# Kernel optimization log

Hardware: AMD Instinct MI355X
Metric: run time of the kernel (lower is better)

The kernel has to match this reference:

```python
import jax, jax.numpy as jnp
import numpy as np
from functools import partial

H = 128  # GRU hidden size
L = 16   # dim_latents


def _gru_dir(x_tbd, W_ih, W_hh, b_ih, b_hh):
    """Single-direction GRU over time-major input x_tbd [T,B,D] -> [T,B,H].
    Torch gate order: r, z, n."""
    T, B, _ = x_tbd.shape
    # Precompute input projections for all timesteps: [T,B,3H]
    xp = jnp.einsum('tbd,gd->tbg', x_tbd, W_ih) + b_ih
    h0 = jnp.zeros((B, H), dtype=x_tbd.dtype)

    def step(h, xp_t):
        gh = h @ W_hh.T + b_hh            # [B,3H]
        xr, xz, xn = jnp.split(xp_t, 3, axis=-1)
        hr, hz, hn = jnp.split(gh, 3, axis=-1)
        r = jax.nn.sigmoid(xr + hr)
        z = jax.nn.sigmoid(xz + hz)
        n = jnp.tanh(xn + r * hn)
        h_new = (1.0 - z) * n + z * h
        return h_new, h_new

    _, ys = jax.lax.scan(step, h0, xp)
    return ys  # [T,B,H]


def setup_inputs() -> dict:
    key = jax.random.key(0)
    ks = jax.random.split(key, 8)
    B, T, N = 256, 1000, 256
    s_ih = 1.0 / np.sqrt(N)
    s_hh = 1.0 / np.sqrt(H)
    s_fc = 1.0 / np.sqrt(2 * H + L)
    return {
        'y_aux': jax.random.normal(ks[0], (B, T, N), dtype=jnp.float32),
        'W_ih_fwd': jax.random.normal(ks[1], (3 * H, N), dtype=jnp.float32) * s_ih,
        'W_hh_fwd': jax.random.normal(ks[2], (3 * H, H), dtype=jnp.float32) * s_hh,
        'b_ih_fwd': jnp.zeros((3 * H,), dtype=jnp.float32),
        'b_hh_fwd': jnp.zeros((3 * H,), dtype=jnp.float32),
        'W_ih_bwd': jax.random.normal(ks[3], (3 * H, N), dtype=jnp.float32) * s_ih,
        'W_hh_bwd': jax.random.normal(ks[4], (3 * H, H), dtype=jnp.float32) * s_hh,
        'b_ih_bwd': jnp.zeros((3 * H,), dtype=jnp.float32),
        'b_hh_bwd': jnp.zeros((3 * H,), dtype=jnp.float32),
        'W_mu': jax.random.normal(ks[5], (L, 2 * H + L), dtype=jnp.float32) * s_fc,
        'b_mu': jnp.zeros((L,), dtype=jnp.float32),
        'W_lv': jax.random.normal(ks[6], (L, 2 * H + L), dtype=jnp.float32) * s_fc,
        'b_lv': jnp.zeros((L,), dtype=jnp.float32),
    }


def reference(y_aux, W_ih_fwd, W_hh_fwd, b_ih_fwd, b_hh_fwd,
              W_ih_bwd, W_hh_bwd, b_ih_bwd, b_hh_bwd,
              W_mu, b_mu, W_lv, b_lv):
    # [B,T,N] -> time-major [T,B,N]
    x = jnp.transpose(y_aux, (1, 0, 2))
    out_f = _gru_dir(x, W_ih_fwd, W_hh_fwd, b_ih_fwd, b_hh_fwd)
    out_b = _gru_dir(x[::-1], W_ih_bwd, W_hh_bwd, b_ih_bwd, b_hh_bwd)[::-1]
    rnn_output = jnp.concatenate([out_f, out_b], axis=-1)  # [T,B,2H]
    # hn[0]: bidirectional hidden states at t=0
    hn0 = rnn_output[0]                                    # [B,2H]
    B = hn0.shape[0]
    temp = jnp.concatenate([jnp.zeros((B, L), dtype=hn0.dtype), hn0], axis=1)
    mu_0 = temp @ W_mu.T + b_mu
    log_var_0 = temp @ W_lv.T + b_lv
    return (mu_0, log_var_0, rnn_output)
```

## Files before the change

kernel.cpp:

```cpp
#include <hip/hip_runtime.h>
#include <hip/hip_bf16.h>

typedef short bf16x8 __attribute__((ext_vector_type(8)));
typedef float f32x4  __attribute__((ext_vector_type(4)));

#define TSTEPS 1000
#define BATCH  256
#define NIN    256
#define HID    128
#define TC     50
#define LOG2E  1.44269504088896f

#define GIDX_N 8192
#define XP4_ELEMS (2ull*TSTEPS*GIDX_N)
#define XP2_OFF_BYTES (XP4_ELEMS*16ull)
#define XP_NEED (XP4_ELEMS*16ull + 2ull*TSTEPS*GIDX_N*8ull)

__device__ __forceinline__ ushort f2bf(float f){
  union { float f; unsigned u; } v; v.f = f;
  unsigned r = v.u + 0x7fffu + ((v.u >> 16) & 1u);
  return (ushort)(r >> 16);
}
__device__ __forceinline__ uint pk2(float lo, float hi){
  __hip_bfloat162 h = __float22bfloat162_rn(make_float2(lo, hi));
  union { __hip_bfloat162 h; uint u; } c; c.h = h; return c.u;
}
__device__ __forceinline__ float bflo(uint w){ union{uint u;float f;}c; c.u = w<<16; return c.f; }
__device__ __forceinline__ float bfhi(uint w){ union{uint u;float f;}c; c.u = w & 0xffff0000u; return c.f; }

__device__ __forceinline__ float sigmoid_fast(float x){
  return __builtin_amdgcn_rcpf(1.f + __expf(-x));
}
__device__ __forceinline__ float tanh_fast(float a){
  const float e = __expf(2.f*fabsf(a));
  const float t = fmaf(-2.f, __builtin_amdgcn_rcpf(e + 1.f), 1.f);
  return copysignf(t, a);
}
__device__ __forceinline__ bf16x8 ld_w8(const float* p){
  union { uint u[4]; bf16x8 v; } c;
  c.u[0]=pk2(p[0],p[1]); c.u[1]=pk2(p[2],p[3]);
  c.u[2]=pk2(p[4],p[5]); c.u[3]=pk2(p[6],p[7]);
  return c.v;
}
__device__ __forceinline__ bf16x8 ld_w8s(const float* p, float s){
  union { uint u[4]; bf16x8 v; } c;
  c.u[0]=pk2(p[0]*s,p[1]*s); c.u[1]=pk2(p[2]*s,p[3]*s);
  c.u[2]=pk2(p[4]*s,p[5]*s); c.u[3]=pk2(p[6]*s,p[7]*s);
  return c.v;
}

__global__ __launch_bounds__(512) void xp_gemm(
    const float* __restrict__ y_aux,
    const float* __restrict__ Wf, const float* __restrict__ bihf, const float* __restrict__ bhhf,
    const float* __restrict__ Wb, const float* __restrict__ bihb, const float* __restrict__ bhhb,
    uint4* __restrict__ xp4, uint2* __restrict__ xp2)
{
  const int nch = TSTEPS/TC;
  const int blk = blockIdx.x;
  const int dir = blk / (16*nch);
  const int rem = blk % (16*nch);
  const int btile = rem / nch;
  const int tch = rem % nch;
  const int b0 = btile*16;
  const int tid=threadIdx.x, wave=tid>>6, lane=tid&63, lrow=lane&15, lgrp=lane>>4;
  const float* Wih = dir? Wb : Wf;
  const float* bih = dir? bihb : bihf;
  const float* bhh = dir? bhhb : bhhf;

  __shared__ __align__(16) ushort xsh[2][16][264];

  bf16x8 wf[3][8];
  f32x4 cinit[3];
  #pragma unroll
  for (int t3=0;t3<3;++t3){
    const int g = t3*128 + wave*16 + lrow;
    #pragma unroll
    for (int kk=0;kk<8;++kk)
      wf[t3][kk] = ld_w8s(Wih + g*NIN + kk*32 + lgrp*8, LOG2E);
    const float bv = LOG2E * (bih[g] + (t3<2 ? bhh[g] : 0.f));
    cinit[t3][0]=bv; cinit[t3][1]=bv; cinit[t3][2]=bv; cinit[t3][3]=bv;
  }

  const int row = tid>>5, f8 = tid&31;
  const float* xsrc = y_aux + (size_t)(b0+row)*(TSTEPS*NIN) + (size_t)(tch*TC)*NIN + f8*8;
  {
    float4 a = *(const float4*)xsrc;
    float4 b = *(const float4*)(xsrc+4);
    union{uint u[4]; bf16x8 v;} c;
    c.u[0]=pk2(a.x,a.y); c.u[1]=pk2(a.z,a.w); c.u[2]=pk2(b.x,b.y); c.u[3]=pk2(b.z,b.w);
    *(bf16x8*)&xsh[0][row][f8*8] = c.v;
  }
  float4 Aa = *(const float4*)(xsrc + 1*NIN), Ab = *(const float4*)(xsrc + 1*NIN + 4);
  float4 Ba = *(const float4*)(xsrc + 2*NIN), Bb = *(const float4*)(xsrc + 2*NIN + 4);
  __syncthreads();

  size_t sidx = ((size_t)dir*TSTEPS + (size_t)(tch*TC))*GIDX_N
              + (size_t)((btile*8 + wave)*64 + lane);

  for (int k=0;k<TC;k+=2){
    {
      f32x4 a0=cinit[0], a1=cinit[1], a2=cinit[2];
      #pragma unroll
      for (int kk=0;kk<8;++kk){
        bf16x8 a = *(const bf16x8*)&xsh[0][lrow][kk*32 + lgrp*8];
        a0 = __builtin_amdgcn_mfma_f32_16x16x32_bf16(a, wf[0][kk], a0, 0,0,0);
        a1 = __builtin_amdgcn_mfma_f32_16x16x32_bf16(a, wf[1][kk], a1, 0,0,0);
        a2 = __builtin_amdgcn_mfma_f32_16x16x32_bf16(a, wf[2][kk], a2, 0,0,0);
      }
      uint4 o4; o4.x=pk2(a0[0],a0[1]); o4.y=pk2(a0[2],a0[3]);
                o4.z=pk2(a1[0],a1[1]); o4.w=pk2(a1[2],a1[3]);
      uint2 o2; o2.x=pk2(a2[0],a2[1]); o2.y=pk2(a2[2],a2[3]);
      xp4[sidx]=o4; xp2[sidx]=o2; sidx += GIDX_N;
      union{uint u[4]; bf16x8 v;} c;
      c.u[0]=pk2(Aa.x,Aa.y); c.u[1]=pk2(Aa.z,Aa.w); c.u[2]=pk2(Ab.x,Ab.y); c.u[3]=pk2(Ab.z,Ab.w);
      *(bf16x8*)&xsh[1][row][f8*8] = c.v;
      const int t3 = (k+3 <= TC-1) ? (k+3) : (TC-1);
      Aa = *(const float4*)(xsrc + (size_t)t3*NIN);
      Ab = *(const float4*)(xsrc + (size_t)t3*NIN + 4);
      asm volatile("s_waitcnt lgkmcnt(0)\n\ts_barrier" ::: "memory");
    }
    {
      f32x4 a0=cinit[0], a1=cinit[1], a2=cinit[2];
      #pragma unroll
      for (int kk=0;kk<8;++kk){
        bf16x8 a = *(const bf16x8*)&xsh[1][lrow][kk*32 + lgrp*8];
        a0 = __builtin_amdgcn_mfma_f32_16x16x32_bf16(a, wf[0][kk], a0, 0,0,0);
        a1 = __builtin_amdgcn_mfma_f32_16x16x32_bf16(a, wf[1][kk], a1, 0,0,0);
        a2 = __builtin_amdgcn_mfma_f32_16x16x32_bf16(a, wf[2][kk], a2, 0,0,0);
      }
      uint4 o4; o4.x=pk2(a0[0],a0[1]); o4.y=pk2(a0[2],a0[3]);
                o4.z=pk2(a1[0],a1[1]); o4.w=pk2(a1[2],a1[3]);
      uint2 o2; o2.x=pk2(a2[0],a2[1]); o2.y=pk2(a2[2],a2[3]);
      xp4[sidx]=o4; xp2[sidx]=o2; sidx += GIDX_N;
      union{uint u[4]; bf16x8 v;} c;
      c.u[0]=pk2(Ba.x,Ba.y); c.u[1]=pk2(Ba.z,Ba.w); c.u[2]=pk2(Bb.x,Bb.y); c.u[3]=pk2(Bb.z,Bb.w);
      *(bf16x8*)&xsh[0][row][f8*8] = c.v;
      const int t4 = (k+4 <= TC-1) ? (k+4) : (TC-1);
      Ba = *(const float4*)(xsrc + (size_t)t4*NIN);
      Bb = *(const float4*)(xsrc + (size_t)t4*NIN + 4);
      asm volatile("s_waitcnt lgkmcnt(0)\n\ts_barrier" ::: "memory");
    }
  }
}

__global__ __launch_bounds__(512) void gru_rec(
    const uint4* __restrict__ xp4, const uint2* __restrict__ xp2,
    const float* __restrict__ Whhf, const float* __restrict__ bhhf,
    const float* __restrict__ Whhb, const float* __restrict__ bhhb,
    float* __restrict__ out)
{
  const int blk=blockIdx.x, dir=blk>>4, btile=blk&15, b0=btile<<4;
  const int tid=threadIdx.x, wave=tid>>6, lane=tid&63, lrow=lane&15, lgrp=lane>>4;
  const float* Whh = dir? Whhb : Whhf;
  const float* bhh = dir? bhhb : bhhf;

  __shared__ __align__(16) ushort hbuf[2][16][136];

  bf16x8 whh[3][4];
  #pragma unroll
  for (int t3=0;t3<3;++t3){
    const int g = t3*128 + wave*16 + lrow;
    #pragma unroll
    for (int kk=0;kk<4;++kk)
      whh[t3][kk] = ld_w8s(Whh + g*HID + kk*32 + lgrp*8, LOG2E);
  }
  const int hcol = wave*16 + lrow;
  const float bh2s = LOG2E * bhh[256 + hcol];

  { ushort* hb=&hbuf[0][0][0]; for (int i=tid;i<16*136;i+=512) hb[i]=0; }

  const int tt0 = dir? (TSTEPS-1):0;
  const long long d4 = dir? -(long long)GIDX_N : (long long)GIDX_N;
  const size_t gbase = ((size_t)dir*TSTEPS + (size_t)tt0)*GIDX_N
                     + (size_t)((btile*8+wave)*64+lane);
  const uint4* q4p = xp4 + gbase;
  const uint2* q2p = xp2 + gbase;
  uint4 q40 = q4p[0], q41 = q4p[d4];
  uint2 q20 = q2p[0], q21 = q2p[d4];
  const uint4* f4 = q4p + 2*d4;
  const uint2* f2 = q2p + 2*d4;

  float* op = out + 8192 + (size_t)tt0*(BATCH*2*HID)
            + (size_t)(b0 + lgrp*4)*(2*HID) + dir*HID + hcol;
  const long long odel = dir? -(long long)(BATCH*2*HID) : (long long)(BATCH*2*HID);

  float hm[4]={0,0,0,0};
  __syncthreads();

  for (int s=0;s<TSTEPS;++s){
    const int cur=s&1, nxt=cur^1;
    uint4 q42 = *f4; f4 += d4;
    uint2 q22 = *f2; f2 += d4;

    f32x4 ar={0,0,0,0}, az={0,0,0,0}, an={0,0,0,0};
    #pragma unroll
    for (int kk=0;kk<4;++kk){
      bf16x8 a = *(const bf16x8*)&hbuf[cur][lrow][kk*32 + lgrp*8];
      ar = __builtin_amdgcn_mfma_f32_16x16x32_bf16(a, whh[0][kk], ar, 0,0,0);
      az = __builtin_amdgcn_mfma_f32_16x16x32_bf16(a, whh[1][kk], az, 0,0,0);
      an = __builtin_amdgcn_mfma_f32_16x16x32_bf16(a, whh[2][kk], an, 0,0,0);
    }

    float hv[4];
    {
      const float xr[4] = {bflo(q40.x),bfhi(q40.x),bflo(q40.y),bfhi(q40.y)};
      const float xz[4] = {bflo(q40.z),bfhi(q40.z),bflo(q40.w),bfhi(q40.w)};
      const float xn[4] = {bflo(q20.x),bfhi(q20.x),bflo(q20.y),bfhi(q20.y)};
      #pragma unroll
      for (int i=0;i<4;++i){
        const float r = __builtin_amdgcn_rcpf(1.f + __builtin_amdgcn_exp2f(-(ar[i]+xr[i])));
        const float z = __builtin_amdgcn_rcpf(1.f + __builtin_amdgcn_exp2f(-(az[i]+xz[i])));
        const float y  = fmaf(r, an[i]+bh2s, xn[i]);
        const float y2 = y + y;
        const float e  = __builtin_amdgcn_exp2f(fabsf(y2));
        const float t  = fmaf(-2.f, __builtin_amdgcn_rcpf(e+1.f), 1.f);
        const float n  = copysignf(t, y);
        hv[i] = fmaf(z, hm[i]-n, n);
        hm[i] = hv[i];
      }
    }
    const uint p01 = pk2(hv[0],hv[1]);
    const uint p23 = pk2(hv[2],hv[3]);
    hbuf[nxt][lgrp*4+0][hcol] = (ushort)p01;
    hbuf[nxt][lgrp*4+1][hcol] = (ushort)(p01>>16);
    hbuf[nxt][lgrp*4+2][hcol] = (ushort)p23;
    hbuf[nxt][lgrp*4+3][hcol] = (ushort)(p23>>16);
    op[0]   = hv[0];
    op[256] = hv[1];
    op[512] = hv[2];
    op[768] = hv[3];
    op += odel;
    q40=q41; q41=q42; q20=q21; q21=q22;
    asm volatile("s_waitcnt lgkmcnt(0)\n\ts_barrier" ::: "memory");
  }
}

__global__ __launch_bounds__(512) void gru_fused(
    const float* __restrict__ y_aux,
    const float* __restrict__ W_ih_f, const float* __restrict__ W_hh_f,
    const float* __restrict__ b_ih_f, const float* __restrict__ b_hh_f,
    const float* __restrict__ W_ih_b, const float* __restrict__ W_hh_b,
    const float* __restrict__ b_ih_b, const float* __restrict__ b_hh_b,
    float* __restrict__ out)
{
  const int blk  = blockIdx.x;
  const int dir  = blk >> 4;
  const int b0   = (blk & 15) << 4;
  const int tid  = threadIdx.x;
  const int wave = tid >> 6;
  const int lane = tid & 63;
  const int lrow = lane & 15;
  const int lgrp = lane >> 4;

  const float* Wih = dir ? W_ih_b : W_ih_f;
  const float* Whh = dir ? W_hh_b : W_hh_f;
  const float* bih = dir ? b_ih_b : b_ih_f;
  const float* bhh = dir ? b_hh_b : b_hh_f;

  __shared__ __align__(16) ushort hbuf[2][16][136];
  __shared__ __align__(16) ushort xbuf[2][16][264];

  bf16x8 wih_f[3][8];
  bf16x8 whh_f[3][4];
  #pragma unroll
  for (int t3 = 0; t3 < 3; ++t3){
    const int g = t3*128 + wave*16 + lrow;
    #pragma unroll
    for (int kk = 0; kk < 8; ++kk) wih_f[t3][kk] = ld_w8(Wih + g*NIN + kk*32 + lgrp*8);
    #pragma unroll
    for (int kk = 0; kk < 4; ++kk) whh_f[t3][kk] = ld_w8(Whh + g*HID + kk*32 + lgrp*8);
  }
  float bihv[3], bhhv[3];
  #pragma unroll
  for (int t3 = 0; t3 < 3; ++t3){
    const int g = t3*128 + wave*16 + lrow;
    bihv[t3] = bih[g];
    bhhv[t3] = bhh[g];
  }

  for (int i = tid; i < 2*16*136; i += 512) ((ushort*)hbuf)[i] = 0;
  {
    const int row = tid >> 5, f8 = tid & 31;
    const int t0  = dir ? (TSTEPS-1) : 0;
    const float* p = y_aux + (size_t)(b0+row)*(TSTEPS*NIN) + (size_t)t0*NIN + f8*8;
    union{uint u[4]; bf16x8 v;} c;
    float4 a = *(const float4*)p; float4 b = *(const float4*)(p+4);
    c.u[0]=pk2(a.x,a.y); c.u[1]=pk2(a.z,a.w); c.u[2]=pk2(b.x,b.y); c.u[3]=pk2(b.z,b.w);
    *(bf16x8*)&xbuf[0][row][f8*8] = c.v;
  }
  __syncthreads();

  float hm[4] = {0.f, 0.f, 0.f, 0.f};
  const int hcol = wave*16 + lrow;
  float* outr = out + 8192;

  for (int s = 0; s < TSTEPS; ++s){
    const int tt  = dir ? (TSTEPS-1-s) : s;
    const int cur = s & 1, nxt = cur ^ 1;
    const int tn   = dir ? (tt-1) : (tt+1);
    const int prow = tid >> 5, pf8 = tid & 31;
    const bool more = (s < TSTEPS-1);
    float4 pa, pb;
    if (more){
      const float* p = y_aux + (size_t)(b0+prow)*(TSTEPS*NIN) + (size_t)tn*NIN + pf8*8;
      pa = *(const float4*)p;
      pb = *(const float4*)(p+4);
    }

    f32x4 a_rh = {0,0,0,0}, a_zh = {0,0,0,0}, a_nh = {0,0,0,0};
    f32x4 a_rx = {0,0,0,0}, a_zx = {0,0,0,0}, a_nx = {0,0,0,0};
    #pragma unroll
    for (int kk = 0; kk < 4; ++kk){
      bf16x8 a = *(const bf16x8*)&hbuf[cur][lrow][kk*32 + lgrp*8];
      a_rh = __builtin_amdgcn_mfma_f32_16x16x32_bf16(a, whh_f[0][kk], a_rh, 0,0,0);
      a_zh = __builtin_amdgcn_mfma_f32_16x16x32_bf16(a, whh_f[1][kk], a_zh, 0,0,0);
      a_nh = __builtin_amdgcn_mfma_f32_16x16x32_bf16(a, whh_f[2][kk], a_nh, 0,0,0);
    }
    #pragma unroll
    for (int kk = 0; kk < 8; ++kk){
      bf16x8 a = *(const bf16x8*)&xbuf[cur][lrow][kk*32 + lgrp*8];
      a_rx = __builtin_amdgcn_mfma_f32_16x16x32_bf16(a, wih_f[0][kk], a_rx, 0,0,0);
      a_zx = __builtin_amdgcn_mfma_f32_16x16x32_bf16(a, wih_f[1][kk], a_zx, 0,0,0);
      a_nx = __builtin_amdgcn_mfma_f32_16x16x32_bf16(a, wih_f[2][kk], a_nx, 0,0,0);
    }

    #pragma unroll
    for (int i = 0; i < 4; ++i){
      const float rp  = a_rh[i] + a_rx[i] + bihv[0] + bhhv[0];
      const float zp  = a_zh[i] + a_zx[i] + bihv[1] + bhhv[1];
      const float hnp = a_nh[i] + bhhv[2];
      const float xnp = a_nx[i] + bihv[2];
      const float r = sigmoid_fast(rp);
      const float z = sigmoid_fast(zp);
      const float n = tanh_fast(fmaf(r, hnp, xnp));
      const float hv = n + z*(hm[i] - n);
      hm[i] = hv;
      outr[(size_t)tt*(BATCH*2*HID) + (size_t)(b0 + lgrp*4 + i)*(2*HID)
           + dir*HID + hcol] = hv;
      hbuf[nxt][lgrp*4 + i][hcol] = f2bf(hv);
    }

    if (more){
      union{uint u[4]; bf16x8 v;} c;
      c.u[0]=pk2(pa.x,pa.y); c.u[1]=pk2(pa.z,pa.w); c.u[2]=pk2(pb.x,pb.y); c.u[3]=pk2(pb.z,pb.w);
      *(bf16x8*)&xbuf[nxt][prow][pf8*8] = c.v;
    }
    __syncthreads();
  }
}

__global__ void heads(const float* __restrict__ out_rnn,
    const float* __restrict__ W_mu, const float* __restrict__ b_mu,
    const float* __restrict__ W_lv, const float* __restrict__ b_lv,
    float* __restrict__ out)
{
  const int oid   = blockIdx.x*256 + threadIdx.x;
  const int which = oid >> 12;
  const int r     = oid & 4095;
  const int b = r >> 4, j = r & 15;
  const float* W    = which ? W_lv : W_mu;
  const float* bias = which ? b_lv : b_mu;
  const float* h = out_rnn + b*256;
  const float* w = W + j*272 + 16;
  float acc = bias[j];
  for (int c = 0; c < 256; c += 4){
    acc += h[c]*w[c] + h[c+1]*w[c+1] + h[c+2]*w[c+2] + h[c+3]*w[c+3];
  }
  out[(which << 12) + r] = acc;
}

extern "C" void kernel_launch(void* const* d_in, const int* in_sizes, int n_in,
                              void* d_out, int out_size, void* d_ws, size_t ws_size,
                              hipStream_t stream)
{
  const float* y    = (const float*)d_in[0];
  const float* Wihf = (const float*)d_in[1];
  const float* Whhf = (const float*)d_in[2];
  const float* bihf = (const float*)d_in[3];
  const float* bhhf = (const float*)d_in[4];
  const float* Wihb = (const float*)d_in[5];
  const float* Whhb = (const float*)d_in[6];
  const float* bihb = (const float*)d_in[7];
  const float* bhhb = (const float*)d_in[8];
  const float* Wmu  = (const float*)d_in[9];
  const float* bmu  = (const float*)d_in[10];
  const float* Wlv  = (const float*)d_in[11];
  const float* blv  = (const float*)d_in[12];
  float* out = (float*)d_out;

  if (ws_size >= (size_t)XP_NEED){
    uint4* xp4 = (uint4*)d_ws;
    uint2* xp2 = (uint2*)((char*)d_ws + XP2_OFF_BYTES);
    xp_gemm<<<dim3(2*16*(TSTEPS/TC)), dim3(512), 0, stream>>>(
        y, Wihf, bihf, bhhf, Wihb, bihb, bhhb, xp4, xp2);
    gru_rec<<<dim3(32), dim3(512), 0, stream>>>(
        xp4, xp2, Whhf, bhhf, Whhb, bhhb, out);
  } else {
    gru_fused<<<dim3(32), dim3(512), 0, stream>>>(
        y, Wihf, Whhf, bihf, bhhf, Wihb, Whhb, bihb, bhhb, out);
  }
  heads<<<dim3(32), dim3(256), 0, stream>>>(out + 8192, Wmu, bmu, Wlv, blv, out);
}
```

Before: 908.8 us.

## Load GEMM A-operand directly from global into registers, drop LDS staging

The input-projection GEMM kernel no longer stages each timestep's x tile through shared memory with barriers. Each lane now loads its own MFMA A-fragment straight from global memory, prefetches the next timestep into registers, and converts to bf16 in place. The time chunk is halved, which doubles the number of blocks. This removes LDS traffic and the per-step barriers, but it costs more registers and makes each wave read the same x rows redundantly, since all 8 waves load identical data.

After: 1.255 ms. +38.1%, slower.

```diff
diff --git a/kernel.cpp b/kernel.cpp
--- a/kernel.cpp
+++ b/kernel.cpp
@@ -8,7 +8,7 @@
 #define BATCH  256
 #define NIN    256
 #define HID    128
-#define TC     50
+#define TC     25
 #define LOG2E  1.44269504088896f
 
 #define GIDX_N 8192
@@ -67,8 +67,6 @@
   const float* bih = dir? bihb : bihf;
   const float* bhh = dir? bhhb : bhhf;
 
-  __shared__ __align__(16) ushort xsh[2][16][264];
-
   bf16x8 wf[3][8];
   f32x4 cinit[3];
   #pragma unroll
@@ -81,65 +79,46 @@
     cinit[t3][0]=bv; cinit[t3][1]=bv; cinit[t3][2]=bv; cinit[t3][3]=bv;
   }
 
-  const int row = tid>>5, f8 = tid&31;
-  const float* xsrc = y_aux + (size_t)(b0+row)*(TSTEPS*NIN) + (size_t)(tch*TC)*NIN + f8*8;
-  {
-    float4 a = *(const float4*)xsrc;
-    float4 b = *(const float4*)(xsrc+4);
-    union{uint u[4]; bf16x8 v;} c;
-    c.u[0]=pk2(a.x,a.y); c.u[1]=pk2(a.z,a.w); c.u[2]=pk2(b.x,b.y); c.u[3]=pk2(b.z,b.w);
-    *(bf16x8*)&xsh[0][row][f8*8] = c.v;
-  }
-  float4 Aa = *(const float4*)(xsrc + 1*NIN), Ab = *(const float4*)(xsrc + 1*NIN + 4);
-  float4 Ba = *(const float4*)(xsrc + 2*NIN), Bb = *(const float4*)(xsrc + 2*NIN + 4);
-  __syncthreads();
-
+  const float* xbase = y_aux + (size_t)(b0+lrow)*(TSTEPS*NIN)
+                     + (size_t)(tch*TC)*NIN + lgrp*8;
   size_t sidx = ((size_t)dir*TSTEPS + (size_t)(tch*TC))*GIDX_N
               + (size_t)((btile*8 + wave)*64 + lane);
 
-  for (int k=0;k<TC;k+=2){
-    {
-      f32x4 a0=cinit[0], a1=cinit[1], a2=cinit[2];
-      #pragma unroll
-      for (int kk=0;kk<8;++kk){
-        bf16x8 a = *(const bf16x8*)&xsh[0][lrow][kk*32 + lgrp*8];
-        a0 = __builtin_amdgcn_mfma_f32_16x16x32_bf16(a, wf[0][kk], a0, 0,0,0);
-        a1 = __builtin_amdgcn_mfma_f32_16x16x32_bf16(a, wf[1][kk], a1, 0,0,0);
-        a2 = __builtin_amdgcn_mfma_f32_16x16x32_bf16(a, wf[2][kk], a2, 0,0,0);
-      }
-      uint4 o4; o4.x=pk2(a0[0],a0[1]); o4.y=pk2(a0[2],a0[3]);
-                o4.z=pk2(a1[0],a1[1]); o4.w=pk2(a1[2],a1[3]);
-      uint2 o2; o2.x=pk2(a2[0],a2[1]); o2.y=pk2(a2[2],a2[3]);
-      xp4[sidx]=o4; xp2[sidx]=o2; sidx += GIDX_N;
+  float4 pa[8], pb[8];
+  #pragma unroll
+  for (int kk=0;kk<8;++kk){
+    const float* p = xbase + kk*32;
+    pa[kk] = *(const float4*)p;
+    pb[kk] = *(const float4*)(p+4);
+  }
+
+  for (int k=0;k<TC;++k){
+    bf16x8 a[8];
+    #pragma unroll
+    for (int kk=0;kk<8;++kk){
       union{uint u[4]; bf16x8 v;} c;
-      c.u[0]=pk2(Aa.x,Aa.y); c.u[1]=pk2(Aa.z,Aa.w); c.u[2]=pk2(Ab.x,Ab.y); c.u[3]=pk2(Ab.z,Ab.w);
-      *(bf16x8*)&xsh[1][row][f8*8] = c.v;
-      const int t3 = (k+3 <= TC-1) ? (k+3) : (TC-1);
-      Aa = *(const float4*)(xsrc + (size_t)t3*NIN);
-      Ab = *(const float4*)(xsrc + (size_t)t3*NIN + 4);
-      asm volatile("s_waitcnt lgkmcnt(0)\n\ts_barrier" ::: "memory");
-    }
-    {
-      f32x4 a0=cinit[0], a1=cinit[1], a2=cinit[2];
-      #pragma unroll
-      for (int kk=0;kk<8;++kk){
-        bf16x8 a = *(const bf16x8*)&xsh[1][lrow][kk*32 + lgrp*8];
-        a0 = __builtin_amdgcn_mfma_f32_16x16x32_bf16(a, wf[0][kk], a0, 0,0,0);
-        a1 = __builtin_amdgcn_mfma_f32_16x16x32_bf16(a, wf[1][kk], a1, 0,0,0);
-        a2 = __builtin_amdgcn_mfma_f32_16x16x32_bf16(a, wf[2][kk], a2, 0,0,0);
-      }
-      uint4 o4; o4.x=pk2(a0[0],a0[1]); o4.y=pk2(a0[2],a0[3]);
-                o4.z=pk2(a1[0],a1[1]); o4.w=pk2(a1[2],a1[3]);
-      uint2 o2; o2.x=pk2(a2[0],a2[1]); o2.y=pk2(a2[2],a2[3]);
-      xp4[sidx]=o4; xp2[sidx]=o2; sidx += GIDX_N;
-      union{uint u[4]; bf16x8 v;} c;
-      c.u[0]=pk2(Ba.x,Ba.y); c.u[1]=pk2(Ba.z,Ba.w); c.u[2]=pk2(Bb.x,Bb.y); c.u[3]=pk2(Bb.z,Bb.w);
-      *(bf16x8*)&xsh[0][row][f8*8] = c.v;
-      const int t4 = (k+4 <= TC-1) ? (k+4) : (TC-1);
-      Ba = *(const float4*)(xsrc + (size_t)t4*NIN);
-      Bb = *(const float4*)(xsrc + (size_t)t4*NIN + 4);
-      asm volatile("s_waitcnt lgkmcnt(0)\n\ts_barrier" ::: "memory");
-    }
+      c.u[0]=pk2(pa[kk].x,pa[kk].y); c.u[1]=pk2(pa[kk].z,pa[kk].w);
+      c.u[2]=pk2(pb[kk].x,pb[kk].y); c.u[3]=pk2(pb[kk].z,pb[kk].w);
+      a[kk] = c.v;
+    }
+    const int tn = (k+1 < TC) ? (k+1) : (TC-1);
+    const float* pn = xbase + (size_t)tn*NIN;
+    #pragma unroll
+    for (int kk=0;kk<8;++kk){
+      pa[kk] = *(const float4*)(pn + kk*32);
+      pb[kk] = *(const float4*)(pn + kk*32 + 4);
+    }
+    f32x4 a0=cinit[0], a1=cinit[1], a2=cinit[2];
+    #pragma unroll
+    for (int kk=0;kk<8;++kk){
+      a0 = __builtin_amdgcn_mfma_f32_16x16x32_bf16(a[kk], wf[0][kk], a0, 0,0,0);
+      a1 = __builtin_amdgcn_mfma_f32_16x16x32_bf16(a[kk], wf[1][kk], a1, 0,0,0);
+      a2 = __builtin_amdgcn_mfma_f32_16x16x32_bf16(a[kk], wf[2][kk], a2, 0,0,0);
+    }
+    uint4 o4; o4.x=pk2(a0[0],a0[1]); o4.y=pk2(a0[2],a0[3]);
+              o4.z=pk2(a1[0],a1[1]); o4.w=pk2(a1[2],a1[3]);
+    uint2 o2; o2.x=pk2(a2[0],a2[1]); o2.y=pk2(a2[2],a2[3]);
+    xp4[sidx]=o4; xp2[sidx]=o2; sidx += GIDX_N;
   }
 }
 
```
